# Optimization experiments

Hardware: AMD Instinct MI355X
Metric: run time of the kernel (lower is better)

The kernel has to match this reference:

```python
import jax, jax.numpy as jnp
import numpy as np

DIM = 256
BATCH = 131072


def setup_inputs() -> dict:
    key = jax.random.key(0)
    kx, kl, ku = jax.random.split(key, 3)
    x = jax.random.normal(kx, (BATCH, DIM), dtype=jnp.float32)
    # l: unit lower-triangular (eye + strict lower random), as in __init__
    l = jnp.eye(DIM, dtype=jnp.float32) + jnp.tril(
        jax.random.normal(kl, (DIM, DIM), dtype=jnp.float32), -1)
    # u: unit upper-triangular (eye + strict upper random)
    u = jnp.eye(DIM, dtype=jnp.float32) + jnp.triu(
        jax.random.normal(ku, (DIM, DIM), dtype=jnp.float32), 1)
    # p: fixed random permutation matrix (buffer, not trained)
    perm = np.random.RandomState(0).permutation(DIM)
    p = jnp.zeros((DIM, DIM), dtype=jnp.float32).at[
        np.arange(DIM), perm].set(1.0)
    return {"x": x, "p": p, "l": l, "u": u}


def reference(x, p, l, u):
    # forward (reverse=False): w = p @ l @ u ; y = (w @ x.T).T = x @ w.T
    w = p @ l @ u                      # [dim, dim]
    y = x @ w.T                        # [batch, dim]
    # log|det(w)| = log|det(u)| since p is a permutation (|det|=1) and l is
    # unit-triangular; u is upper-triangular so det(u) = prod(diag(u)).
    log_det = jnp.sum(jnp.log(jnp.abs(jnp.diag(u))))
    return (y, log_det)
```

## Files before the change

kernel.cpp:

```cpp
#include <hip/hip_runtime.h>

#define DIM 256
#define BATCH 131072
#define BM 64
#define NT 8

typedef __attribute__((ext_vector_type(8))) short s16x8;
typedef __attribute__((ext_vector_type(8))) unsigned short u16x8;
typedef __attribute__((ext_vector_type(4))) float f32x4;

static __device__ __forceinline__ unsigned short f2bf(float f) {
    unsigned int u = __builtin_bit_cast(unsigned int, f);
    u = (u + 0x7FFFu + ((u >> 16) & 1u)) >> 16;
    return (unsigned short)u;
}

static __device__ __forceinline__ s16x8 cvt8(const float4 a, const float4 b) {
    return (s16x8){ (short)f2bf(a.x), (short)f2bf(a.y), (short)f2bf(a.z), (short)f2bf(a.w),
                    (short)f2bf(b.x), (short)f2bf(b.y), (short)f2bf(b.z), (short)f2bf(b.w) };
}

__global__ void lu_perm(const float* __restrict__ l, const float* __restrict__ u,
                        const float* __restrict__ p, unsigned short* __restrict__ wpk) {
    __shared__ float sL[DIM];
    __shared__ int dest;
    const int i = blockIdx.x, j = threadIdx.x;
    sL[j] = l[i * DIM + j];
    if (p[j * DIM + i] != 0.0f) dest = j;
    __syncthreads();
    float s0 = 0.f, s1 = 0.f, s2 = 0.f, s3 = 0.f;
    #pragma unroll 4
    for (int k = 0; k < DIM; k += 4) {
        s0 = fmaf(sL[k + 0], u[(k + 0) * DIM + j], s0);
        s1 = fmaf(sL[k + 1], u[(k + 1) * DIM + j], s1);
        s2 = fmaf(sL[k + 2], u[(k + 2) * DIM + j], s2);
        s3 = fmaf(sL[k + 3], u[(k + 3) * DIM + j], s3);
    }
    const int d = dest;
    const int idx = ((d >> 4) * 8 + (j >> 5)) * 512 + (((j >> 3) & 3) * 16 + (d & 15)) * 8 + (j & 7);
    wpk[idx] = f2bf((s0 + s1) + (s2 + s3));
}

__global__ void logdet_kernel(const float* __restrict__ u, float* __restrict__ out) {
    const int i = threadIdx.x;
    float v = logf(fabsf(u[i * DIM + i]));
    #pragma unroll
    for (int o = 32; o; o >>= 1) v += __shfl_down(v, o, 64);
    __shared__ float partial[4];
    if ((i & 63) == 0) partial[i >> 6] = v;
    __syncthreads();
    if (i == 0) out[0] = (partial[0] + partial[1]) + (partial[2] + partial[3]);
}

__global__ __launch_bounds__(256, 3) void gemm_xwT(const float* __restrict__ x,
                                                   const unsigned short* __restrict__ wpk,
                                                   float* __restrict__ y) {
    __shared__ unsigned short sA[2][BM * 32];

    const int t    = threadIdx.x;
    const int lane = t & 63;
    const int wc   = t >> 6;
    const int lr   = lane & 15;
    const int lg   = lane >> 4;
    const long row0 = (long)blockIdx.x * BM;

    const int sr = t >> 2;
    const int sc = (t & 3) * 8;
    const float* asrc = x + (row0 + sr) * DIM + sc;
    unsigned short* adst = &sA[0][(sr >> 4) * 512 + ((t & 3) * 16 + (sr & 15)) * 8];
    const int bufoff = BM * 32;

    const unsigned short* bbase = wpk + (wc * 4) * 8 * 512 + lane * 8;

    f32x4 acc[4][4];
    #pragma unroll
    for (int mi = 0; mi < 4; mi++)
        #pragma unroll
        for (int n = 0; n < 4; n++) acc[mi][n] = (f32x4){0.f, 0.f, 0.f, 0.f};

    float4 sa0 = *(const float4*)(asrc);
    float4 sa1 = *(const float4*)(asrc + 4);
    float4 sb0 = *(const float4*)(asrc + 32);
    float4 sb1 = *(const float4*)(asrc + 36);
    s16x8 bf0[4], bf1[4];
    #pragma unroll
    for (int n = 0; n < 4; n++)
        bf0[n] = __builtin_bit_cast(s16x8, *(const u16x8*)(bbase + (n * 8 + 0) * 512));
    *(s16x8*)adst = cvt8(sa0, sa1);
    __syncthreads();

    #pragma unroll
    for (int ks = 0; ks < NT; ++ks) {
        if (ks < NT - 2) {
            const float* nsrc = asrc + (ks + 2) * 32;
            if ((ks & 1) == 0) { sa0 = *(const float4*)(nsrc); sa1 = *(const float4*)(nsrc + 4); }
            else               { sb0 = *(const float4*)(nsrc); sb1 = *(const float4*)(nsrc + 4); }
        }
        if (ks < NT - 1) {
            #pragma unroll
            for (int n = 0; n < 4; n++) {
                const s16x8 v = __builtin_bit_cast(s16x8, *(const u16x8*)(bbase + (n * 8 + ks + 1) * 512));
                if ((ks & 1) == 0) bf1[n] = v; else bf0[n] = v;
            }
        }
        const unsigned short* abuf = &sA[0][(ks & 1) * bufoff];
        s16x8 af[4];
        #pragma unroll
        for (int mi = 0; mi < 4; mi++)
            af[mi] = *(const s16x8*)(abuf + mi * 512 + lane * 8);
        #pragma unroll
        for (int mi = 0; mi < 4; mi++)
            #pragma unroll
            for (int n = 0; n < 4; n++)
                acc[mi][n] = __builtin_amdgcn_mfma_f32_16x16x32_bf16(
                    af[mi], (ks & 1) ? bf1[n] : bf0[n], acc[mi][n], 0, 0, 0);
        if (ks < NT - 1) {
            unsigned short* wdst = adst + ((ks + 1) & 1) * bufoff;
            *(s16x8*)wdst = ((ks & 1) == 0) ? cvt8(sb0, sb1) : cvt8(sa0, sa1);
        }
        __syncthreads();
    }

    #pragma unroll
    for (int mi = 0; mi < 4; mi++) {
        const long gr0 = row0 + mi * 16 + lg * 4;
        #pragma unroll
        for (int n = 0; n < 4; n++) {
            const int gc = wc * 64 + n * 16 + lr;
            #pragma unroll
            for (int j = 0; j < 4; j++)
                y[(gr0 + j) * DIM + gc] = acc[mi][n][j];
        }
    }
}

extern "C" void kernel_launch(void* const* d_in, const int* in_sizes, int n_in,
                              void* d_out, int out_size, void* d_ws, size_t ws_size,
                              hipStream_t stream) {
    const float* x = (const float*)d_in[0];
    const float* p = (const float*)d_in[1];
    const float* l = (const float*)d_in[2];
    const float* u = (const float*)d_in[3];
    float* out = (float*)d_out;

    unsigned short* wpk = (unsigned short*)d_ws;

    lu_perm<<<DIM, DIM, 0, stream>>>(l, u, p, wpk);
    logdet_kernel<<<1, DIM, 0, stream>>>(u, out + (size_t)BATCH * DIM);
    gemm_xwT<<<BATCH / BM, 256, 0, stream>>>(x, wpk, out);
}
```

Before: 66.76 us.

## Preload full A tile into swizzled LDS and stage epilogue stores through LDS

The GEMM kernel now loads and converts the whole 64x256 A tile into LDS up front, using an XOR swizzle to reduce bank conflicts. This removes the per-k-step double buffering and the barrier inside the loop. The output is written through a padded LDS staging buffer per wave, so global stores become coalesced float4 rows instead of scattered scalar stores. The cost is a larger LDS footprint (32KB), which may lower occupancy, and the loads are no longer overlapped with MFMA work.

Result: faster. 62.94 us (-5.7%).

```diff
diff --git a/kernel.cpp b/kernel.cpp
--- a/kernel.cpp
+++ b/kernel.cpp
@@ -3,7 +3,6 @@
 #define DIM 256
 #define BATCH 131072
 #define BM 64
-#define NT 8
 
 typedef __attribute__((ext_vector_type(8))) short s16x8;
 typedef __attribute__((ext_vector_type(8))) unsigned short u16x8;
@@ -55,7 +54,7 @@
 __global__ __launch_bounds__(256, 3) void gemm_xwT(const float* __restrict__ x,
                                                    const unsigned short* __restrict__ wpk,
                                                    float* __restrict__ y) {
-    __shared__ unsigned short sA[2][BM * 32];
+    __shared__ unsigned short sA[4 * 8 * 512];
 
     const int t    = threadIdx.x;
     const int lane = t & 63;
@@ -64,13 +63,21 @@
     const int lg   = lane >> 4;
     const long row0 = (long)blockIdx.x * BM;
 
-    const int sr = t >> 2;
-    const int sc = (t & 3) * 8;
-    const float* asrc = x + (row0 + sr) * DIM + sc;
-    unsigned short* adst = &sA[0][(sr >> 4) * 512 + ((t & 3) * 16 + (sr & 15)) * 8];
-    const int bufoff = BM * 32;
+    const int sr  = t >> 2;
+    const int kq  = t & 3;
+    const int r15 = sr & 15;
+    const int mb  = t >> 6;
+    const float* asrc = x + (row0 + sr) * DIM + kq * 8;
+    const int lpx = (kq * 16 + r15) ^ (kq << 1);
+    #pragma unroll
+    for (int q = 0; q < 8; ++q) {
+        const float4 v0 = *(const float4*)(asrc + q * 32);
+        const float4 v1 = *(const float4*)(asrc + q * 32 + 4);
+        *(s16x8*)&sA[(mb * 8 + q) * 512 + (lpx ^ q) * 8] = cvt8(v0, v1);
+    }
 
-    const unsigned short* bbase = wpk + (wc * 4) * 8 * 512 + lane * 8;
+    const unsigned short* bbase = wpk + wc * 4 * 8 * 512 + lane * 8;
+    const int lx = lane ^ ((lane >> 4) << 1);
 
     f32x4 acc[4][4];
     #pragma unroll
@@ -78,58 +85,48 @@
         #pragma unroll
         for (int n = 0; n < 4; n++) acc[mi][n] = (f32x4){0.f, 0.f, 0.f, 0.f};
 
-    float4 sa0 = *(const float4*)(asrc);
-    float4 sa1 = *(const float4*)(asrc + 4);
-    float4 sb0 = *(const float4*)(asrc + 32);
-    float4 sb1 = *(const float4*)(asrc + 36);
-    s16x8 bf0[4], bf1[4];
+    s16x8 bf[2][4];
     #pragma unroll
     for (int n = 0; n < 4; n++)
-        bf0[n] = __builtin_bit_cast(s16x8, *(const u16x8*)(bbase + (n * 8 + 0) * 512));
-    *(s16x8*)adst = cvt8(sa0, sa1);
+        bf[0][n] = __builtin_bit_cast(s16x8, *(const u16x8*)(bbase + n * 8 * 512));
+
     __syncthreads();
 
     #pragma unroll
-    for (int ks = 0; ks < NT; ++ks) {
-        if (ks < NT - 2) {
-            const float* nsrc = asrc + (ks + 2) * 32;
-            if ((ks & 1) == 0) { sa0 = *(const float4*)(nsrc); sa1 = *(const float4*)(nsrc + 4); }
-            else               { sb0 = *(const float4*)(nsrc); sb1 = *(const float4*)(nsrc + 4); }
+    for (int ks = 0; ks < 8; ++ks) {
+        if (ks < 7) {
+            #pragma unroll
+            for (int n = 0; n < 4; n++)
+                bf[(ks + 1) & 1][n] = __builtin_bit_cast(s16x8,
+                    *(const u16x8*)(bbase + (n * 8 + ks + 1) * 512));
         }
-        if (ks < NT - 1) {
-            #pragma unroll
-            for (int n = 0; n < 4; n++) {
-                const s16x8 v = __builtin_bit_cast(s16x8, *(const u16x8*)(bbase + (n * 8 + ks + 1) * 512));
-                if ((ks & 1) == 0) bf1[n] = v; else bf0[n] = v;
-            }
-        }
-        const unsigned short* abuf = &sA[0][(ks & 1) * bufoff];
         s16x8 af[4];
         #pragma unroll
         for (int mi = 0; mi < 4; mi++)
-            af[mi] = *(const s16x8*)(abuf + mi * 512 + lane * 8);
+            af[mi] = *(const s16x8*)&sA[(mi * 8 + ks) * 512 + (lx ^ ks) * 8];
         #pragma unroll
         for (int mi = 0; mi < 4; mi++)
             #pragma unroll
             for (int n = 0; n < 4; n++)
                 acc[mi][n] = __builtin_amdgcn_mfma_f32_16x16x32_bf16(
-                    af[mi], (ks & 1) ? bf1[n] : bf0[n], acc[mi][n], 0, 0, 0);
-        if (ks < NT - 1) {
-            unsigned short* wdst = adst + ((ks + 1) & 1) * bufoff;
-            *(s16x8*)wdst = ((ks & 1) == 0) ? cvt8(sb0, sb1) : cvt8(sa0, sa1);
-        }
-        __syncthreads();
+                    af[mi], bf[ks & 1][n], acc[mi][n], 0, 0, 0);
     }
 
+    __syncthreads();
+
+    float* ep = (float*)sA + wc * 1088;
     #pragma unroll
-    for (int mi = 0; mi < 4; mi++) {
-        const long gr0 = row0 + mi * 16 + lg * 4;
+    for (int mi = 0; mi < 4; ++mi) {
         #pragma unroll
-        for (int n = 0; n < 4; n++) {
-            const int gc = wc * 64 + n * 16 + lr;
+        for (int n = 0; n < 4; n++)
             #pragma unroll
             for (int j = 0; j < 4; j++)
-                y[(gr0 + j) * DIM + gc] = acc[mi][n][j];
+                ep[(lg * 4 + j) * 68 + n * 16 + lr] = acc[mi][n][j];
+        #pragma unroll
+        for (int it = 0; it < 4; ++it) {
+            const int row = it * 4 + lg;
+            const float4 v = *(const float4*)&ep[row * 68 + lr * 4];
+            *(float4*)&y[(row0 + mi * 16 + row) * DIM + wc * 64 + lr * 4] = v;
         }
     }
 }
```
